# Optimization experiments

Measured on AMD Instinct MI355X. Metric: run time of the kernel, lower is better.

Reference implementation:

```python
import jax, jax.numpy as jnp
import numpy as np
from math import factorial, sqrt

LMAX = 2
NB = 32
NRBF = 20
CUTOFF = 5.0
N_ATOMS = 20000
N_EDGES = 400000
T = 2
M = (LMAX + 1) ** 2
LIDX = np.repeat(np.arange(LMAX + 1), 2 * np.arange(LMAX + 1) + 1)  # l of each flat (l,m) index


def _cg_complex(j1, m1, j2, m2, j3, m3):
    # Racah formula for complex-SH Clebsch-Gordan coefficients
    if m3 != m1 + m2 or j3 < abs(j1 - j2) or j3 > j1 + j2:
        return 0.0
    f = factorial
    pref = sqrt((2 * j3 + 1) * f(j1 + j2 - j3) * f(j1 - j2 + j3) * f(-j1 + j2 + j3) / f(j1 + j2 + j3 + 1))
    pref *= sqrt(f(j1 + m1) * f(j1 - m1) * f(j2 + m2) * f(j2 - m2) * f(j3 + m3) * f(j3 - m3))
    kmin = max(0, j2 - j3 - m1, j1 + m2 - j3)
    kmax = min(j1 + j2 - j3, j1 - m1, j2 + m2)
    s = 0.0
    for k in range(kmin, kmax + 1):
        s += (-1) ** k / (f(k) * f(j1 + j2 - j3 - k) * f(j1 - m1 - k) * f(j2 + m2 - k) * f(j3 - j2 + m1 + k) * f(j3 - j1 - m2 + k))
    return pref * s


def _u_matrix(l):
    # real-SH = U @ complex-SH (rows: real m from -l..l, cols: complex m')
    U = np.zeros((2 * l + 1, 2 * l + 1), dtype=np.complex128)
    for m in range(-l, l + 1):
        if m == 0:
            U[l, l] = 1.0
        elif m > 0:
            U[l + m, l + m] = (-1) ** m / sqrt(2)
            U[l + m, l - m] = 1.0 / sqrt(2)
        else:
            mu = -m
            U[l + m, l + m] = 1j / sqrt(2)
            U[l + m, l - m] = -1j * (-1) ** mu / sqrt(2)
    return U


def _build_cg_rsh(lmax):
    # CG coefficients in the real-SH basis, parity invariant (odd l1+l2+l3 blocks zero)
    cg = np.zeros((M, M, M), dtype=np.float64)
    Us = [_u_matrix(l) for l in range(lmax + 1)]
    for l1 in range(lmax + 1):
        for l2 in range(lmax + 1):
            for l3 in range(lmax + 1):
                if (l1 + l2 + l3) % 2 == 1 or l3 < abs(l1 - l2) or l3 > l1 + l2:
                    continue
                Cc = np.zeros((2 * l1 + 1, 2 * l2 + 1, 2 * l3 + 1), dtype=np.complex128)
                for i, m1 in enumerate(range(-l1, l1 + 1)):
                    for j, m2 in enumerate(range(-l2, l2 + 1)):
                        m3 = m1 + m2
                        if abs(m3) <= l3:
                            Cc[i, j, l3 + m3] = _cg_complex(l1, m1, l2, m2, l3, m3)
                R = np.einsum('ai,bj,ck,ijk->abc', Us[l1], Us[l2], np.conj(Us[l3]), Cc)
                cg[l1 * l1:(l1 + 1) ** 2, l2 * l2:(l2 + 1) ** 2, l3 * l3:(l3 + 1) ** 2] = np.real(R)
    return cg.astype(np.float32)


CG = jnp.asarray(_build_cg_rsh(LMAX))   # [9, 9, 9]
LIDX_J = jnp.asarray(LIDX)


def _rsh(dirs):
    # real spherical harmonics up to l=2 on unit vectors, flat (l,m) order -> [P, 9]
    x, y, z = dirs[:, 0], dirs[:, 1], dirs[:, 2]
    c1 = 0.4886025119029199
    c2 = 1.0925484305920792
    return jnp.stack([
        jnp.full_like(x, 0.28209479177387814),
        c1 * y, c1 * z, c1 * x,
        c2 * x * y, c2 * y * z,
        0.31539156525252005 * (3.0 * z * z - 1.0),
        c2 * x * z,
        0.5462742152960396 * (x * x - y * y),
    ], axis=1)


def _forward(atomic_numbers, r_ij, idx_i, idx_j, emb, Wf, bf, Wm1, Wm2, Wm3, Wg, bg):
    d = jnp.linalg.norm(r_ij, axis=1)                      # [P]
    Y = _rsh(r_ij / d[:, None])                            # [P, 9]
    offsets = jnp.linspace(0.0, CUTOFF, NRBF)
    width = CUTOFF / (NRBF - 1)
    radial = jnp.exp(-0.5 / width ** 2 * (d[:, None] - offsets) ** 2)   # GaussianRBF [P, NRBF]
    fcut = jnp.where(d < CUTOFF, 0.5 * (jnp.cos(d * jnp.pi / CUTOFF) + 1.0), 0.0)  # CosineCutoff
    x0 = emb[atomic_numbers]                               # nuclear embedding [N, NB]
    x = jnp.concatenate([x0[:, None, :], jnp.zeros((x0.shape[0], M - 1, NB), x0.dtype)], axis=1)  # scalar2rsh
    for t in range(T):
        # SO3Convolution: per-edge radial filter per output degree l, cutoff gated
        Wl = ((radial @ Wf[t].T + bf[t]) * fcut[:, None]).reshape(-1, LMAX + 1, NB)
        xj = x[idx_j]                                      # gather neighbors [P, 9, NB]
        tbc = jnp.einsum('pa,abc->pbc', Y, CG)             # contract Y_ij with CG
        yij = jnp.einsum('pbc,pbn->pcn', tbc, xj) * Wl[:, LIDX_J, :]
        dx = jax.ops.segment_sum(yij, idx_i, num_segments=x.shape[0], indices_are_sorted=True)
        ddx = jnp.einsum('xcn,kn->xck', dx, Wm1[t])        # mixing1 (no bias)
        dx = dx + jnp.einsum('abc,xan,xbn->xcn', CG, dx, ddx)  # SO3TensorProduct
        dx = jnp.einsum('xcn,kn->xck', dx, Wm2[t])         # mixing2
        h = jax.nn.sigmoid((dx[:, 0, :] @ Wg[t].T + bg[t]).reshape(-1, LMAX + 1, NB))
        dx = dx * h[:, LIDX_J, :]                          # SO3ParametricGatedNonlinearity
        dx = jnp.einsum('xcn,kn->xck', dx, Wm3[t])         # mixing3
        x = x + dx
    return x                                               # multipole representation [N, 9, NB]


def setup_inputs():
    key = jax.random.key(0)
    ks = jax.random.split(key, 12)
    return {
        'atomic_numbers': jax.random.randint(ks[0], (N_ATOMS,), 1, 100),
        'r_ij': jax.random.normal(ks[1], (N_EDGES, 3), jnp.float32),
        'idx_i': jnp.sort(jax.random.randint(ks[2], (N_EDGES,), 0, N_ATOMS)),
        'idx_j': jax.random.randint(ks[3], (N_EDGES,), 0, N_ATOMS),
        'emb': jax.random.normal(ks[4], (101, NB), jnp.float32).at[0].set(0.0),
        'Wf': jax.random.normal(ks[5], (T, (LMAX + 1) * NB, NRBF), jnp.float32) / sqrt(NRBF),
        'bf': jnp.zeros((T, (LMAX + 1) * NB), jnp.float32),
        'Wm1': jax.random.normal(ks[6], (T, NB, NB), jnp.float32) / sqrt(NB),
        'Wm2': jax.random.normal(ks[7], (T, NB, NB), jnp.float32) / sqrt(NB),
        'Wm3': jax.random.normal(ks[8], (T, NB, NB), jnp.float32) / sqrt(NB),
        'Wg': jax.random.normal(ks[9], (T, (LMAX + 1) * NB, NB), jnp.float32) / sqrt(NB),
        'bg': jnp.zeros((T, (LMAX + 1) * NB), jnp.float32),
    }


def reference(atomic_numbers, r_ij, idx_i, idx_j, emb, Wf, bf, Wm1, Wm2, Wm3, Wg, bg):
    return _forward(atomic_numbers, r_ij, idx_i, idx_j, emb, Wf, bf, Wm1, Wm2, Wm3, Wg, bg)
```

## Files before the change

kernel.cpp:

```cpp
#include <hip/hip_runtime.h>

#define CHUNK 16

constexpr double CFACT[8] = {1.,1.,2.,6.,24.,120.,720.,5040.};

constexpr double csqrt(double x){
  if (x <= 0.0) return 0.0;
  double s = 1.0;
  while (x > 4.0)  { x *= 0.25; s *= 2.0; }
  while (x < 0.25) { x *= 4.0;  s *= 0.5; }
  double g = 1.0;
  for (int i=0;i<10;i++) g = 0.5*(g + x/g);
  return s*g;
}

constexpr double cg_complex(int j1,int m1,int j2,int m2,int j3,int m3){
  if (m3 != m1+m2 || j3 < (j1>j2?j1-j2:j2-j1) || j3 > j1+j2) return 0.0;
  double pref = csqrt((2.0*j3+1.0)*CFACT[j1+j2-j3]*CFACT[j1-j2+j3]*CFACT[-j1+j2+j3]/CFACT[j1+j2+j3+1]);
  pref *= csqrt(CFACT[j1+m1]*CFACT[j1-m1]*CFACT[j2+m2]*CFACT[j2-m2]*CFACT[j3+m3]*CFACT[j3-m3]);
  int kmin = 0;
  if (j2-j3-m1 > kmin) kmin = j2-j3-m1;
  if (j1+m2-j3 > kmin) kmin = j1+m2-j3;
  int kmax = j1+j2-j3;
  if (j1-m1 < kmax) kmax = j1-m1;
  if (j2+m2 < kmax) kmax = j2+m2;
  double s = 0.0;
  for (int k=kmin;k<=kmax;++k){
    double t = 1.0/(CFACT[k]*CFACT[j1+j2-j3-k]*CFACT[j1-m1-k]*CFACT[j2+m2-k]*CFACT[j3-j2+m1+k]*CFACT[j3-j1-m2+k]);
    s += (k&1)? -t : t;
  }
  return pref*s;
}

struct UR { int n; int mc[2]; double re[2]; double im[2]; };
constexpr UR u_row(int m){
  UR u{}; const double is2 = 0.70710678118654752440;
  if (m==0){ u.n=1; u.mc[0]=0; u.re[0]=1.0; u.im[0]=0.0; u.mc[1]=0; u.re[1]=0.0; u.im[1]=0.0; }
  else if (m>0){ u.n=2; u.mc[0]=m;  u.re[0]=((m&1)? -is2:is2); u.im[0]=0.0;
                        u.mc[1]=-m; u.re[1]=is2;               u.im[1]=0.0; }
  else { int mu=-m; u.n=2; u.mc[0]=m;  u.re[0]=0.0; u.im[0]=is2;
                           u.mc[1]=mu; u.re[1]=0.0; u.im[1]=((mu&1)? is2:-is2); }
  return u;
}

struct CGTab { float v[9][9][9]; };
constexpr CGTab build_cg(){
  CGTab g{};
  double cc[9][9][9] = {};
  for (int a=0;a<9;a++){
    int l1 = (a==0)?0:((a<4)?1:2); int m1 = a - (l1*l1+l1);
    for (int b=0;b<9;b++){
      int l2 = (b==0)?0:((b<4)?1:2); int m2 = b - (l2*l2+l2);
      int m3 = m1+m2;
      for (int l3=0;l3<=2;l3++){
        if (m3 < -l3 || m3 > l3) continue;
        cc[a][b][l3*l3+l3+m3] = cg_complex(l1,m1,l2,m2,l3,m3);
      }
    }
  }
  for (int l1=0;l1<=2;l1++) for (int l2=0;l2<=2;l2++) for (int l3=0;l3<=2;l3++){
    if (((l1+l2+l3)&1)==1) continue;
    int dl = (l1>l2)?(l1-l2):(l2-l1);
    if (l3 < dl || l3 > l1+l2) continue;
    for (int m1=-l1;m1<=l1;m1++) for (int m2=-l2;m2<=l2;m2++) for (int m3=-l3;m3<=l3;m3++){
      UR ua = u_row(m1), ub = u_row(m2), uc = u_row(m3);
      double acc = 0.0;
      for (int i=0;i<ua.n;i++) for (int j=0;j<ub.n;j++){
        double zr = ua.re[i]*ub.re[j] - ua.im[i]*ub.im[j];
        double zi = ua.re[i]*ub.im[j] + ua.im[i]*ub.re[j];
        for (int k=0;k<uc.n;k++){
          double rp = zr*uc.re[k] + zi*uc.im[k];
          if (rp != 0.0)
            acc += rp * cc[l1*l1+l1+ua.mc[i]][l2*l2+l2+ub.mc[j]][l3*l3+l3+uc.mc[k]];
        }
      }
      g.v[l1*l1+l1+m1][l2*l2+l2+m2][l3*l3+l3+m3] = (float)acc;
    }
  }
  return g;
}
constexpr CGTab CGT = build_cg();

template<bool FIRST>
__global__ __launch_bounds__(256) void edge_kernel(
    const float* __restrict__ r_ij, const int* __restrict__ idx_i, const int* __restrict__ idx_j,
    const float* __restrict__ x, const int* __restrict__ Z, const float* __restrict__ emb,
    const float* __restrict__ Wf_t, const float* __restrict__ bf_t,
    float* __restrict__ dx, int n_edges)
{
  int tid = threadIdx.x;
  int g = tid >> 5, lane = tid & 31;

  int base = (blockIdx.x*8 + g)*CHUNK;
  if (base >= n_edges) return;

  int pidx;
  {
    int e0 = base + (lane & 15);
    if (e0 > n_edges-1) e0 = n_edges-1;
    pidx = (lane < 16) ? idx_i[e0] : idx_j[e0];
  }

  float wfr[3][20]; float bfl[3];
  #pragma unroll
  for (int l=0;l<3;l++){
    const float* rp = Wf_t + (l*32+lane)*20;
    #pragma unroll
    for (int q=0;q<5;q++){
      float4 v4 = *reinterpret_cast<const float4*>(rp + q*4);
      wfr[l][q*4+0]=v4.x; wfr[l][q*4+1]=v4.y; wfr[l][q*4+2]=v4.z; wfr[l][q*4+3]=v4.w;
    }
    bfl[l] = bf_t[l*32+lane];
  }

  const float STEP  = 5.0f/19.0f;
  const float ALPHA = -0.5f/(STEP*STEP);
  float myoff = (float)lane * STEP;

  float racc[9];
  #pragma unroll
  for (int c=0;c<9;c++) racc[c]=0.f;
  int cur_i = -1;

  float xjn[9]; float xjn0; float rnx, rny, rnz;
  {
    int j0 = __shfl(pidx, 16, 32);
    if (FIRST){
      xjn0 = emb[Z[j0]*32 + lane];
    } else {
      const float* xp = x + j0*288 + lane;
      #pragma unroll
      for (int b=0;b<9;b++) xjn[b] = xp[b*32];
    }
    rnx = r_ij[base*3+0]; rny = r_ij[base*3+1]; rnz = r_ij[base*3+2];
  }

  #pragma unroll 1
  for (int k=0;k<CHUNK;k++){
    int e = base + k;
    if (e >= n_edges) break;

    float rx = rnx, ry = rny, rz = rnz;
    float xj[9]; float xj0;
    if (FIRST){
      xj0 = xjn0;
    } else {
      #pragma unroll
      for (int b=0;b<9;b++) xj[b] = xjn[b];
    }
    int ii = __shfl(pidx, k, 32);

    if (k+1 < CHUNK && e+1 < n_edges){
      int jn = __shfl(pidx, 16+k+1, 32);
      if (FIRST){
        xjn0 = emb[Z[jn]*32 + lane];
      } else {
        const float* xp = x + jn*288 + lane;
        #pragma unroll
        for (int b=0;b<9;b++) xjn[b] = xp[b*32];
      }
      rnx = r_ij[(e+1)*3+0]; rny = r_ij[(e+1)*3+1]; rnz = r_ij[(e+1)*3+2];
    }

    float d2 = fmaf(rx,rx,fmaf(ry,ry,rz*rz));
    float dd = sqrtf(d2);
    float inv = __fdividef(1.0f, dd);
    float X = rx*inv, Yv = ry*inv, Zv = rz*inv;
    const float c1 = 0.4886025119029199f, c2 = 1.0925484305920792f;
    float Y[9];
    Y[0]=0.28209479177387814f; Y[1]=c1*Yv; Y[2]=c1*Zv; Y[3]=c1*X;
    Y[4]=c2*X*Yv; Y[5]=c2*Yv*Zv; Y[6]=0.31539156525252005f*(3.f*Zv*Zv-1.f);
    Y[7]=c2*X*Zv; Y[8]=0.5462742152960396f*(X*X-Yv*Yv);

    float dtl = dd - myoff;
    float rbl = __expf(ALPHA*dtl*dtl);
    float wl0=bfl[0], wl1=bfl[1], wl2=bfl[2];
    #pragma unroll
    for (int r=0;r<20;r++){
      float rb = __shfl(rbl, r, 32);
      wl0 = fmaf(rb, wfr[0][r], wl0);
      wl1 = fmaf(rb, wfr[1][r], wl1);
      wl2 = fmaf(rb, wfr[2][r], wl2);
    }
    float fc = (dd < 5.0f) ? 0.5f*(__cosf(dd*0.6283185307179586f)+1.0f) : 0.0f;
    wl0*=fc; wl1*=fc; wl2*=fc;

    if (ii != cur_i){
      if (cur_i >= 0){
        float* dp = dx + cur_i*288 + lane;
        #pragma unroll
        for (int c=0;c<9;c++){ atomicAdd(dp + c*32, racc[c]); racc[c]=0.f; }
      }
      cur_i = ii;
    }

    if (FIRST){
      racc[0] = fmaf(wl0, Y[0]*xj0, racc[0]);
      #pragma unroll
      for (int c=1;c<4;c++) racc[c] = fmaf(wl1, Y[c]*xj0, racc[c]);
      #pragma unroll
      for (int c=4;c<9;c++) racc[c] = fmaf(wl2, Y[c]*xj0, racc[c]);
    } else {
      float yv[9];
      #pragma unroll
      for (int c=0;c<9;c++) yv[c]=0.f;
      #pragma unroll
      for (int a=0;a<9;a++){
        #pragma unroll
        for (int b=0;b<9;b++){
          bool any = false;
          #pragma unroll
          for (int c=0;c<9;c++) any = any | (CGT.v[a][b][c] != 0.f);
          if (any){
            float p = Y[a]*xj[b];
            #pragma unroll
            for (int c=0;c<9;c++){
              if (CGT.v[a][b][c] != 0.f) yv[c] = fmaf(CGT.v[a][b][c], p, yv[c]);
            }
          }
        }
      }
      racc[0] = fmaf(wl0, yv[0], racc[0]);
      #pragma unroll
      for (int c=1;c<4;c++) racc[c] = fmaf(wl1, yv[c], racc[c]);
      #pragma unroll
      for (int c=4;c<9;c++) racc[c] = fmaf(wl2, yv[c], racc[c]);
    }
  }
  if (cur_i >= 0){
    float* dp = dx + cur_i*288 + lane;
    #pragma unroll
    for (int c=0;c<9;c++) atomicAdd(dp + c*32, racc[c]);
  }
}

template<bool FIRST, bool LAST>
__global__ __launch_bounds__(256) void atom_kernel(
    float* __restrict__ x, float* __restrict__ dxg,
    const int* __restrict__ Z, const float* __restrict__ emb,
    const float* __restrict__ Wm1_t, const float* __restrict__ Wm2_t, const float* __restrict__ Wm3_t,
    const float* __restrict__ Wg_t, const float* __restrict__ bg_t, int n_atoms)
{
  __shared__ __align__(16) float tile[8][288];
  int tid = threadIdx.x;
  int g = tid>>5, k = tid&31;
  int atom = blockIdx.x*8 + g;
  if (atom >= n_atoms) return;
  float* tg = &tile[g][0];
  const float4* t4 = reinterpret_cast<const float4*>(tg);

  float embv;
  if (FIRST) embv = emb[Z[atom]*32 + k];

  float* dp = dxg + atom*288 + k;
  float v[9];
  #pragma unroll
  for (int c=0;c<9;c++){
    v[c]=dp[c*32]; tg[c*32+k]=v[c];
    if (!LAST) dp[c*32]=0.f;
  }

  float wr[32];
  {
    const float4* w4 = reinterpret_cast<const float4*>(Wm1_t + k*32);
    #pragma unroll
    for (int q=0;q<8;q++){ float4 a=w4[q]; wr[4*q]=a.x; wr[4*q+1]=a.y; wr[4*q+2]=a.z; wr[4*q+3]=a.w; }
  }
  float u[9];
  #pragma unroll
  for (int c=0;c<9;c++){
    float s=0.f;
    #pragma unroll
    for (int q=0;q<8;q++){
      float4 tv = t4[c*8+q];
      s = fmaf(tv.x, wr[4*q+0], s); s = fmaf(tv.y, wr[4*q+1], s);
      s = fmaf(tv.z, wr[4*q+2], s); s = fmaf(tv.w, wr[4*q+3], s);
    }
    u[c]=s;
  }

  float w[9];
  #pragma unroll
  for (int c=0;c<9;c++) w[c]=v[c];
  #pragma unroll
  for (int a=0;a<9;a++){
    #pragma unroll
    for (int b=0;b<9;b++){
      bool any = false;
      #pragma unroll
      for (int c=0;c<9;c++) any = any | (CGT.v[a][b][c] != 0.f);
      if (any){
        float p = v[a]*u[b];
        #pragma unroll
        for (int c=0;c<9;c++){
          if (CGT.v[a][b][c] != 0.f) w[c] = fmaf(CGT.v[a][b][c], p, w[c]);
        }
      }
    }
  }

  #pragma unroll
  for (int c=0;c<9;c++) tg[c*32+k]=w[c];
  {
    const float4* w4 = reinterpret_cast<const float4*>(Wm2_t + k*32);
    #pragma unroll
    for (int q=0;q<8;q++){ float4 a=w4[q]; wr[4*q]=a.x; wr[4*q+1]=a.y; wr[4*q+2]=a.z; wr[4*q+3]=a.w; }
  }
  float p[9];
  #pragma unroll
  for (int c=0;c<9;c++){
    float s=0.f;
    #pragma unroll
    for (int q=0;q<8;q++){
      float4 tv = t4[c*8+q];
      s = fmaf(tv.x, wr[4*q+0], s); s = fmaf(tv.y, wr[4*q+1], s);
      s = fmaf(tv.z, wr[4*q+2], s); s = fmaf(tv.w, wr[4*q+3], s);
    }
    p[c]=s;
  }

  tg[k] = p[0];
  float s0=bg_t[k], s1=bg_t[32+k], s2=bg_t[64+k];
  {
    const float4* wg0 = reinterpret_cast<const float4*>(Wg_t + (     k)*32);
    const float4* wg1 = reinterpret_cast<const float4*>(Wg_t + (32 + k)*32);
    const float4* wg2 = reinterpret_cast<const float4*>(Wg_t + (64 + k)*32);
    #pragma unroll
    for (int q=0;q<8;q++){
      float4 tv = t4[q];
      float4 a0 = wg0[q], a1 = wg1[q], a2 = wg2[q];
      s0 = fmaf(tv.x,a0.x,s0); s0 = fmaf(tv.y,a0.y,s0); s0 = fmaf(tv.z,a0.z,s0); s0 = fmaf(tv.w,a0.w,s0);
      s1 = fmaf(tv.x,a1.x,s1); s1 = fmaf(tv.y,a1.y,s1); s1 = fmaf(tv.z,a1.z,s1); s1 = fmaf(tv.w,a1.w,s1);
      s2 = fmaf(tv.x,a2.x,s2); s2 = fmaf(tv.y,a2.y,s2); s2 = fmaf(tv.z,a2.z,s2); s2 = fmaf(tv.w,a2.w,s2);
    }
  }
  float h0 = 1.f/(1.f+__expf(-s0));
  float h1 = 1.f/(1.f+__expf(-s1));
  float h2 = 1.f/(1.f+__expf(-s2));

  float q9[9];
  q9[0]=p[0]*h0;
  #pragma unroll
  for (int c=1;c<4;c++) q9[c]=p[c]*h1;
  #pragma unroll
  for (int c=4;c<9;c++) q9[c]=p[c]*h2;

  #pragma unroll
  for (int c=0;c<9;c++) tg[c*32+k]=q9[c];
  {
    const float4* w4 = reinterpret_cast<const float4*>(Wm3_t + k*32);
    #pragma unroll
    for (int q=0;q<8;q++){ float4 a=w4[q]; wr[4*q]=a.x; wr[4*q+1]=a.y; wr[4*q+2]=a.z; wr[4*q+3]=a.w; }
  }
  float* xo = x + atom*288 + k;
  #pragma unroll
  for (int c=0;c<9;c++){
    float s=0.f;
    #pragma unroll
    for (int q=0;q<8;q++){
      float4 tv = t4[c*8+q];
      s = fmaf(tv.x, wr[4*q+0], s); s = fmaf(tv.y, wr[4*q+1], s);
      s = fmaf(tv.z, wr[4*q+2], s); s = fmaf(tv.w, wr[4*q+3], s);
    }
    if (FIRST){
      float base = (c==0)? embv : 0.f;
      xo[c*32] = base + s;
    } else {
      xo[c*32] += s;
    }
  }
}

extern "C" void kernel_launch(void* const* d_in, const int* in_sizes, int n_in,
                              void* d_out, int out_size, void* d_ws, size_t ws_size,
                              hipStream_t stream)
{
  const int*   Z    = (const int*)d_in[0];
  const float* r_ij = (const float*)d_in[1];
  const int*   idxi = (const int*)d_in[2];
  const int*   idxj = (const int*)d_in[3];
  const float* emb  = (const float*)d_in[4];
  const float* Wf   = (const float*)d_in[5];
  const float* bf   = (const float*)d_in[6];
  const float* Wm1  = (const float*)d_in[7];
  const float* Wm2  = (const float*)d_in[8];
  const float* Wm3  = (const float*)d_in[9];
  const float* Wg   = (const float*)d_in[10];
  const float* bg   = (const float*)d_in[11];
  int n_atoms = in_sizes[0];
  int n_edges = in_sizes[1]/3;

  float* x  = (float*)d_out;
  float* dx = (float*)d_ws;

  hipMemsetAsync(dx, 0, (size_t)n_atoms*288*sizeof(float), stream);

  int eblocks = (n_edges + 8*CHUNK - 1)/(8*CHUNK);
  int ablocks = (n_atoms + 7)/8;

  edge_kernel<true><<<eblocks,256,0,stream>>>(r_ij, idxi, idxj, x, Z, emb, Wf, bf, dx, n_edges);
  atom_kernel<true,false><<<ablocks,256,0,stream>>>(x, dx, Z, emb, Wm1, Wm2, Wm3, Wg, bg, n_atoms);

  edge_kernel<false><<<eblocks,256,0,stream>>>(r_ij, idxi, idxj, x, Z, emb,
                                        Wf + 96*20, bf + 96, dx, n_edges);
  atom_kernel<false,true><<<ablocks,256,0,stream>>>(x, dx, Z, emb,
                                        Wm1 + 1024, Wm2 + 1024, Wm3 + 1024,
                                        Wg + 96*32, bg + 96, n_atoms);
}
```

Baseline: 440.1 us.

## Swizzle block order across XCDs, preload edge vectors, unroll edge loop

Remaps block indices so consecutive logical blocks land on the same XCD (round-robin dispatch over 8 XCDs), meant to improve L2 locality of the sorted idx_i and atom data. The edge kernel now loads all 16 edges' r_ij coordinates with two coalesced per-lane loads and pulls them out with shuffles instead of issuing scalar loads each iteration. The edge loop is fully unrolled and the bounds check on the prefetch is dropped. The unrolling raises register pressure and code size, and the prefetch can read past the end for the final partial chunk.

```diff
diff --git a/kernel.cpp b/kernel.cpp
--- a/kernel.cpp
+++ b/kernel.cpp
@@ -81,6 +81,12 @@
 }
 constexpr CGTab CGT = build_cg();
 
+__device__ __forceinline__ int swizzle_block(int b, int nb){
+  int P = nb >> 3;
+  if (b < (P<<3)) return (b & 7) * P + (b >> 3);
+  return b;
+}
+
 template<bool FIRST>
 __global__ __launch_bounds__(256) void edge_kernel(
     const float* __restrict__ r_ij, const int* __restrict__ idx_i, const int* __restrict__ idx_j,
@@ -91,7 +97,8 @@
   int tid = threadIdx.x;
   int g = tid >> 5, lane = tid & 31;
 
-  int base = (blockIdx.x*8 + g)*CHUNK;
+  int vb = swizzle_block(blockIdx.x, gridDim.x);
+  int base = (vb*8 + g)*CHUNK;
   if (base >= n_edges) return;
 
   int pidx;
@@ -100,6 +107,14 @@
     if (e0 > n_edges-1) e0 = n_edges-1;
     pidx = (lane < 16) ? idx_i[e0] : idx_j[e0];
   }
+  float rv0, rv1;
+  {
+    long long rmax = (long long)n_edges*3 - 1;
+    long long a0 = (long long)base*3 + lane;       if (a0 > rmax) a0 = rmax;
+    long long a1 = (long long)base*3 + 32 + lane;  if (a1 > rmax) a1 = rmax;
+    rv0 = r_ij[a0];
+    rv1 = r_ij[a1];
+  }
 
   float wfr[3][20]; float bfl[3];
   #pragma unroll
@@ -122,7 +137,7 @@
   for (int c=0;c<9;c++) racc[c]=0.f;
   int cur_i = -1;
 
-  float xjn[9]; float xjn0; float rnx, rny, rnz;
+  float xjn[9]; float xjn0;
   {
     int j0 = __shfl(pidx, 16, 32);
     if (FIRST){
@@ -132,15 +147,13 @@
       #pragma unroll
       for (int b=0;b<9;b++) xjn[b] = xp[b*32];
     }
-    rnx = r_ij[base*3+0]; rny = r_ij[base*3+1]; rnz = r_ij[base*3+2];
-  }
-
-  #pragma unroll 1
+  }
+
+  #pragma unroll
   for (int k=0;k<CHUNK;k++){
     int e = base + k;
     if (e >= n_edges) break;
 
-    float rx = rnx, ry = rny, rz = rnz;
     float xj[9]; float xj0;
     if (FIRST){
       xj0 = xjn0;
@@ -148,9 +161,8 @@
       #pragma unroll
       for (int b=0;b<9;b++) xj[b] = xjn[b];
     }
-    int ii = __shfl(pidx, k, 32);
-
-    if (k+1 < CHUNK && e+1 < n_edges){
+
+    if (k+1 < CHUNK){
       int jn = __shfl(pidx, 16+k+1, 32);
       if (FIRST){
         xjn0 = emb[Z[jn]*32 + lane];
@@ -159,8 +171,13 @@
         #pragma unroll
         for (int b=0;b<9;b++) xjn[b] = xp[b*32];
       }
-      rnx = r_ij[(e+1)*3+0]; rny = r_ij[(e+1)*3+1]; rnz = r_ij[(e+1)*3+2];
-    }
+    }
+
+    int ii = __shfl(pidx, k, 32);
+
+    float rx = (3*k+0 < 32) ? __shfl(rv0, 3*k+0, 32) : __shfl(rv1, 3*k+0-32, 32);
+    float ry = (3*k+1 < 32) ? __shfl(rv0, 3*k+1, 32) : __shfl(rv1, 3*k+1-32, 32);
+    float rz = (3*k+2 < 32) ? __shfl(rv0, 3*k+2, 32) : __shfl(rv1, 3*k+2-32, 32);
 
     float d2 = fmaf(rx,rx,fmaf(ry,ry,rz*rz));
     float dd = sqrtf(d2);
@@ -244,7 +261,8 @@
   __shared__ __align__(16) float tile[8][288];
   int tid = threadIdx.x;
   int g = tid>>5, k = tid&31;
-  int atom = blockIdx.x*8 + g;
+  int vb = swizzle_block(blockIdx.x, gridDim.x);
+  int atom = vb*8 + g;
   if (atom >= n_atoms) return;
   float* tg = &tile[g][0];
   const float4* t4 = reinterpret_cast<const float4*>(tg);
```

Result: faster. 428.9 us (-2.5%).

## Halve edge chunk, preload r_ij via shuffles, specialize CG contraction, fully unroll loop

Applied to the files above, without the earlier changes.

Each wave now handles 8 edges instead of 16. The r_ij coordinates of all edges in the chunk are loaded with a single coalesced per-lane read and then distributed by shuffles, and the Z lookup is hoisted so it is gathered once per lane. The CG tensor product is rewritten to use the Y0 constant and the l=0 output structure, folding identical diagonal coefficients into dot products, and the edge loop is fully unrolled. The goal is fewer dependent scalar loads and fewer FLOPs per edge, at the cost of more blocks, more atomic flushes per edge and higher register pressure from unrolling.

```diff
diff --git a/kernel.cpp b/kernel.cpp
--- a/kernel.cpp
+++ b/kernel.cpp
@@ -1,6 +1,6 @@
 #include <hip/hip_runtime.h>
 
-#define CHUNK 16
+#define CHUNK 8
 
 constexpr double CFACT[8] = {1.,1.,2.,6.,24.,120.,720.,5040.};
 
@@ -81,6 +81,58 @@
 }
 constexpr CGTab CGT = build_cg();
 
+__device__ __forceinline__ void cg_contract(const float* __restrict__ Y,
+                                            const float* __restrict__ xj,
+                                            float* __restrict__ yv){
+  constexpr float Y0 = 0.28209479177387814f;
+  #pragma unroll
+  for (int b=0;b<9;b++) yv[b] = (Y0*CGT.v[0][b][b]) * xj[b];
+  #pragma unroll
+  for (int c=1;c<9;c++){
+    if (CGT.v[c][0][c] == 1.0f) yv[c] = fmaf(Y[c], xj[0], yv[c]);
+    else { float p = Y[c]*xj[0]; yv[c] = fmaf(CGT.v[c][0][c], p, yv[c]); }
+  }
+  if (CGT.v[2][2][0]==CGT.v[1][1][0] && CGT.v[3][3][0]==CGT.v[1][1][0]){
+    float d1 = Y[1]*xj[1]; d1 = fmaf(Y[2],xj[2],d1); d1 = fmaf(Y[3],xj[3],d1);
+    yv[0] = fmaf(CGT.v[1][1][0], d1, yv[0]);
+  } else {
+    #pragma unroll
+    for (int a=1;a<4;a++){ float p=Y[a]*xj[a]; yv[0]=fmaf(CGT.v[a][a][0],p,yv[0]); }
+  }
+  if (CGT.v[5][5][0]==CGT.v[4][4][0] && CGT.v[6][6][0]==CGT.v[4][4][0] &&
+      CGT.v[7][7][0]==CGT.v[4][4][0] && CGT.v[8][8][0]==CGT.v[4][4][0]){
+    float d2 = Y[4]*xj[4];
+    #pragma unroll
+    for (int a=5;a<9;a++) d2 = fmaf(Y[a],xj[a],d2);
+    yv[0] = fmaf(CGT.v[4][4][0], d2, yv[0]);
+  } else {
+    #pragma unroll
+    for (int a=4;a<9;a++){ float p=Y[a]*xj[a]; yv[0]=fmaf(CGT.v[a][a][0],p,yv[0]); }
+  }
+  #pragma unroll
+  for (int a=1;a<9;a++){
+    #pragma unroll
+    for (int b=1;b<9;b++){
+      if (a!=b && CGT.v[a][b][0]!=0.f){ float p=Y[a]*xj[b]; yv[0]=fmaf(CGT.v[a][b][0],p,yv[0]); }
+    }
+  }
+  #pragma unroll
+  for (int a=1;a<9;a++){
+    #pragma unroll
+    for (int b=1;b<9;b++){
+      bool any=false;
+      #pragma unroll
+      for (int c=1;c<9;c++) any = any | (CGT.v[a][b][c]!=0.f);
+      if (any){
+        float p = Y[a]*xj[b];
+        #pragma unroll
+        for (int c=1;c<9;c++)
+          if (CGT.v[a][b][c]!=0.f) yv[c] = fmaf(CGT.v[a][b][c], p, yv[c]);
+      }
+    }
+  }
+}
+
 template<bool FIRST>
 __global__ __launch_bounds__(256) void edge_kernel(
     const float* __restrict__ r_ij, const int* __restrict__ idx_i, const int* __restrict__ idx_j,
@@ -96,9 +148,17 @@
 
   int pidx;
   {
-    int e0 = base + (lane & 15);
+    int e0 = base + (lane & 7);
     if (e0 > n_edges-1) e0 = n_edges-1;
     pidx = (lane < 16) ? idx_i[e0] : idx_j[e0];
+  }
+  int zv = 0;
+  if (FIRST) zv = Z[pidx];
+  float rv0;
+  {
+    long long rmax = (long long)n_edges*3 - 1;
+    long long a0 = (long long)base*3 + lane; if (a0 > rmax) a0 = rmax;
+    rv0 = r_ij[a0];
   }
 
   float wfr[3][20]; float bfl[3];
@@ -122,25 +182,24 @@
   for (int c=0;c<9;c++) racc[c]=0.f;
   int cur_i = -1;
 
-  float xjn[9]; float xjn0; float rnx, rny, rnz;
-  {
-    int j0 = __shfl(pidx, 16, 32);
+  float xjn[9]; float xjn0;
+  {
     if (FIRST){
-      xjn0 = emb[Z[j0]*32 + lane];
+      int z0 = __shfl(zv, 16, 32);
+      xjn0 = emb[z0*32 + lane];
     } else {
+      int j0 = __shfl(pidx, 16, 32);
       const float* xp = x + j0*288 + lane;
       #pragma unroll
       for (int b=0;b<9;b++) xjn[b] = xp[b*32];
     }
-    rnx = r_ij[base*3+0]; rny = r_ij[base*3+1]; rnz = r_ij[base*3+2];
-  }
-
-  #pragma unroll 1
+  }
+
+  #pragma unroll
   for (int k=0;k<CHUNK;k++){
     int e = base + k;
     if (e >= n_edges) break;
 
-    float rx = rnx, ry = rny, rz = rnz;
     float xj[9]; float xj0;
     if (FIRST){
       xj0 = xjn0;
@@ -148,19 +207,24 @@
       #pragma unroll
       for (int b=0;b<9;b++) xj[b] = xjn[b];
     }
-    int ii = __shfl(pidx, k, 32);
-
-    if (k+1 < CHUNK && e+1 < n_edges){
-      int jn = __shfl(pidx, 16+k+1, 32);
+
+    if (k+1 < CHUNK){
       if (FIRST){
-        xjn0 = emb[Z[jn]*32 + lane];
+        int zn = __shfl(zv, 16+k+1, 32);
+        xjn0 = emb[zn*32 + lane];
       } else {
+        int jn = __shfl(pidx, 16+k+1, 32);
         const float* xp = x + jn*288 + lane;
         #pragma unroll
         for (int b=0;b<9;b++) xjn[b] = xp[b*32];
       }
-      rnx = r_ij[(e+1)*3+0]; rny = r_ij[(e+1)*3+1]; rnz = r_ij[(e+1)*3+2];
-    }
+    }
+
+    int ii = __shfl(pidx, k, 32);
+
+    float rx = __shfl(rv0, 3*k+0, 32);
+    float ry = __shfl(rv0, 3*k+1, 32);
+    float rz = __shfl(rv0, 3*k+2, 32);
 
     float d2 = fmaf(rx,rx,fmaf(ry,ry,rz*rz));
     float dd = sqrtf(d2);
@@ -202,24 +266,7 @@
       for (int c=4;c<9;c++) racc[c] = fmaf(wl2, Y[c]*xj0, racc[c]);
     } else {
       float yv[9];
-      #pragma unroll
-      for (int c=0;c<9;c++) yv[c]=0.f;
-      #pragma unroll
-      for (int a=0;a<9;a++){
-        #pragma unroll
-        for (int b=0;b<9;b++){
-          bool any = false;
-          #pragma unroll
-          for (int c=0;c<9;c++) any = any | (CGT.v[a][b][c] != 0.f);
-          if (any){
-            float p = Y[a]*xj[b];
-            #pragma unroll
-            for (int c=0;c<9;c++){
-              if (CGT.v[a][b][c] != 0.f) yv[c] = fmaf(CGT.v[a][b][c], p, yv[c]);
-            }
-          }
-        }
-      }
+      cg_contract(Y, xj, yv);
       racc[0] = fmaf(wl0, yv[0], racc[0]);
       #pragma unroll
       for (int c=1;c<4;c++) racc[c] = fmaf(wl1, yv[c], racc[c]);
```

After: 460.4 us. +4.6%, slower.
